# Kernel tuning notes

Measured on AMD Instinct MI355X. Metric: run time of the kernel, lower is better.

Reference implementation:

```python
import jax, jax.numpy as jnp
import numpy as np

N, D, K_FRAC = 4096, 256, 0.5
EPS = 1e-5  # BatchNorm1d default eps


def setup_inputs() -> dict:
    key = jax.random.key(0)
    kg, kh, kw = jax.random.split(key, 3)
    # sparse binary adjacency with self-loops so all degrees > 0 (pow(D,-1) finite)
    g = (jax.random.uniform(kg, (N, N)) < 0.004).astype(jnp.float32)
    g = jnp.maximum(g, jnp.eye(N, dtype=jnp.float32))
    h = jax.random.normal(kh, (N, D), dtype=jnp.float32)
    return {
        "g": g,
        "h": h,
        "gamma": jnp.ones((D,), jnp.float32),
        "beta": jnp.zeros((D,), jnp.float32),
        "w_proj": jax.random.normal(kw, (D, 1), dtype=jnp.float32) / np.sqrt(D),
        "b_proj": jnp.zeros((1,), jnp.float32),
        "sigma1": jnp.array([0.2], jnp.float32),
    }


def reference(g, h, gamma, beta, w_proj, b_proj, sigma1):
    # BatchNorm1d in training mode: batch statistics over the node axis
    mu = h.mean(0)
    var = h.var(0)  # biased variance, as torch uses for normalization
    h = (h - mu) / jnp.sqrt(var + EPS) * gamma + beta

    deg = g.sum(1)                               # [N] == Z2
    agg = (g @ h) / deg[:, None]                 # diag(D^-1) @ (g @ h), no NxN diag materialized
    Z1 = jnp.abs(h - agg).sum(1)                 # [N]
    pl = jax.nn.sigmoid(Z1 + deg)
    Z3 = (agg @ w_proj + b_proj)[:, 0]           # proj(Z3).squeeze()
    pg = jax.nn.softmax(Z3)                      # 1-D softmax (dim 0)
    pt = jax.nn.sigmoid(pl + pg)
    pf = jax.nn.sigmoid((h @ w_proj + b_proj)[:, 0])
    scores = sigma1[0] * pt + (1.0 - sigma1[0]) * pf

    # top_k_graph
    k = max(2, int(K_FRAC * N))
    _, idx = jax.lax.top_k(scores, k)            # [k]
    h_att = scores[:, None] * h                  # score-weighted features
    un_g = (g != 0).astype(jnp.float32)
    two_hop = ((un_g @ un_g) != 0).astype(jnp.float32)  # binarized 2-hop adjacency
    a_hat = two_hop[idx, :]                      # [k, N] row gather
    new_h = a_hat @ h_att                        # [k, D]
    g_new = a_hat[:, idx]                        # [k, k] column gather
    # norm_g: torch broadcast divides COLUMN j by row-sum degrees[j]
    g_new = g_new / g_new.sum(1)
    return g_new, new_h, idx
```

## Files before the change

### kernel.cpp

```cpp
#include <hip/hip_runtime.h>
#include <math.h>

#define NN 4096
#define DD 256
#define KK 2048
#define NW 64
#define SK 4
#define KC (NN / SK)
#define KW (KC / 32)

typedef float f32x4  __attribute__((ext_vector_type(4)));
typedef short bf16x8 __attribute__((ext_vector_type(8)));

__device__ __forceinline__ int build_list(const unsigned long long* __restrict__ B, int r,
                                          int l, int* cols, int cap) {
    unsigned long long word = B[(size_t)r * NW + l];
    int pc = __popcll(word);
    int off = pc;
    for (int d = 1; d < 64; d <<= 1) {
        int n = __shfl_up(off, d);
        if (l >= d) off += n;
    }
    int total = __shfl(off, 63);
    int base = off - pc;
    while (word) {
        int b = (int)__ffsll(word) - 1;
        word &= word - 1;
        if (base < cap) cols[base] = l * 64 + b;
        ++base;
    }
    return total;
}

__global__ void k_pre(const float* __restrict__ h, const float* __restrict__ g,
                      double* __restrict__ psum, double* __restrict__ psq,
                      unsigned long long* __restrict__ B) {
    int blk = blockIdx.x;
    int t = threadIdx.x;
    if (blk < 64) {
        int d = t;
        int r0 = blk * 64;
        double s0=0,s1=0,s2=0,s3=0,q0=0,q1=0,q2=0,q3=0;
        for (int k = 0; k < 64; k += 4) {
            double x0 = (double)h[(size_t)(r0+k+0) * DD + d];
            double x1 = (double)h[(size_t)(r0+k+1) * DD + d];
            double x2 = (double)h[(size_t)(r0+k+2) * DD + d];
            double x3 = (double)h[(size_t)(r0+k+3) * DD + d];
            s0 += x0; q0 += x0*x0;
            s1 += x1; q1 += x1*x1;
            s2 += x2; q2 += x2*x2;
            s3 += x3; q3 += x3*x3;
        }
        psum[blk * DD + d] = (s0+s1)+(s2+s3);
        psq [blk * DD + d] = (q0+q1)+(q2+q3);
    } else {
        int i = blk - 64;
        int q = t >> 6, l = t & 63;
        const float* gr = g + (size_t)i * NN;
        unsigned long long word = 0ull;
        int lw = l & 15;
        #pragma unroll
        for (int wi = 0; wi < 16; ++wi) {
            float v = gr[(q * 16 + wi) * 64 + l];
            unsigned long long m = __ballot(v != 0.0f);
            if (wi == lw) word = m;
        }
        if (l < 16) B[(size_t)i * NW + q * 16 + l] = word;
    }
}

__global__ void k_stats_final(const double* __restrict__ psum, const double* __restrict__ psq,
                              double* __restrict__ mu, double* __restrict__ rstd) {
    __shared__ double rs[4][DD];
    __shared__ double rq[4][DD];
    int t = threadIdx.x;
    int d = t & (DD - 1);
    int q = t >> 8;
    double s0=0,s1=0,q0=0,q1=0;
    int b0 = q * 16;
    for (int k = 0; k < 16; k += 2) {
        s0 += psum[(b0+k)   * DD + d];
        s1 += psum[(b0+k+1) * DD + d];
        q0 += psq [(b0+k)   * DD + d];
        q1 += psq [(b0+k+1) * DD + d];
    }
    rs[q][d] = s0 + s1;
    rq[q][d] = q0 + q1;
    __syncthreads();
    if (q == 0) {
        double S  = (rs[0][d]+rs[1][d]) + (rs[2][d]+rs[3][d]);
        double Q  = (rq[0][d]+rq[1][d]) + (rq[2][d]+rq[3][d]);
        double m  = S / (double)NN;
        double var = Q / (double)NN - m * m;
        mu[d]   = m;
        rstd[d] = 1.0 / sqrt(var + 1e-5);
    }
}

__global__ void k_main(const float* __restrict__ h, const double* __restrict__ mu,
                       const double* __restrict__ rstd, const float* __restrict__ gamma,
                       const float* __restrict__ beta, const unsigned long long* __restrict__ Bm,
                       const float* __restrict__ w, const float* __restrict__ bp,
                       float* __restrict__ hn, double* __restrict__ zpf,
                       unsigned long long* __restrict__ T, double* __restrict__ Z1,
                       double* __restrict__ Z3, int* __restrict__ degi) {
    __shared__ int cols[4][136];
    int blk = blockIdx.x;
    int t = threadIdx.x;
    int wv = t >> 6, l = t & 63;
    int r = blk * 4 + wv;
    int cnt = build_list(Bm, r, l, cols[wv], 128);
    if (cnt > 128) cnt = 128;
    const float4* h4 = (const float4*)h;
    double s0=0,s1=0,s2=0,s3=0,u0=0,u1=0,u2=0,u3=0;
    unsigned long long a0 = 0ull, a1 = 0ull;
    int j = 0;
    for (; j + 1 < cnt; j += 2) {
        int c0 = cols[wv][j], c1 = cols[wv][j + 1];
        float4 v0 = h4[(size_t)c0 * 64 + l];
        float4 v1 = h4[(size_t)c1 * 64 + l];
        a0 |= Bm[(size_t)c0 * NW + l];
        a1 |= Bm[(size_t)c1 * NW + l];
        s0 += (double)v0.x; s1 += (double)v0.y; s2 += (double)v0.z; s3 += (double)v0.w;
        u0 += (double)v1.x; u1 += (double)v1.y; u2 += (double)v1.z; u3 += (double)v1.w;
    }
    if (j < cnt) {
        int c0 = cols[wv][j];
        float4 v0 = h4[(size_t)c0 * 64 + l];
        a0 |= Bm[(size_t)c0 * NW + l];
        s0 += (double)v0.x; s1 += (double)v0.y; s2 += (double)v0.z; s3 += (double)v0.w;
    }
    T[(size_t)r * NW + l] = a0 | a1;
    s0 += u0; s1 += u1; s2 += u2; s3 += u3;
    const double2* mu2 = (const double2*)mu;
    const double2* rs2 = (const double2*)rstd;
    const float4*  ga4 = (const float4*)gamma;
    const float4*  be4 = (const float4*)beta;
    const float4*  w4  = (const float4*)w;
    double2 mA = mu2[2*l], mB = mu2[2*l+1];
    double2 rA = rs2[2*l], rB = rs2[2*l+1];
    float4 ga = ga4[l], be = be4[l], wl = w4[l];
    double inv = 1.0 / (double)cnt;
    double g0 = (s0 * inv - mA.x) * rA.x * (double)ga.x + (double)be.x;
    double g1 = (s1 * inv - mA.y) * rA.y * (double)ga.y + (double)be.y;
    double g2 = (s2 * inv - mB.x) * rB.x * (double)ga.z + (double)be.z;
    double g3 = (s3 * inv - mB.y) * rB.y * (double)ga.w + (double)be.w;
    float4 hv = h4[(size_t)r * 64 + l];
    double h0 = ((double)hv.x - mA.x) * rA.x * (double)ga.x + (double)be.x;
    double h1 = ((double)hv.y - mA.y) * rA.y * (double)ga.y + (double)be.y;
    double h2 = ((double)hv.z - mB.x) * rB.x * (double)ga.z + (double)be.z;
    double h3 = ((double)hv.w - mB.y) * rB.y * (double)ga.w + (double)be.w;
    float4 o = { (float)h0, (float)h1, (float)h2, (float)h3 };
    ((float4*)hn)[(size_t)r * 64 + l] = o;
    double z1p = (fabs(h0 - g0) + fabs(h1 - g1)) + (fabs(h2 - g2) + fabs(h3 - g3));
    double z3p = (g0 * (double)wl.x + g1 * (double)wl.y)
               + (g2 * (double)wl.z + g3 * (double)wl.w);
    double zfp = (h0 * (double)wl.x + h1 * (double)wl.y)
               + (h2 * (double)wl.z + h3 * (double)wl.w);
    for (int off = 32; off > 0; off >>= 1) {
        z1p += __shfl_down(z1p, off);
        z3p += __shfl_down(z3p, off);
        zfp += __shfl_down(zfp, off);
    }
    if (l == 0) {
        Z1[r] = z1p;
        Z3[r] = z3p + (double)bp[0];
        zpf[r] = zfp + (double)bp[0];
        degi[r] = cnt;
    }
}

__global__ void k_scorekeys(const double* __restrict__ Z1, const double* __restrict__ Z3,
                            const double* __restrict__ zpf, const int* __restrict__ degi,
                            const float* __restrict__ sigma1, float* __restrict__ scores,
                            unsigned long long* __restrict__ keys) {
    __shared__ double red[256];
    int t = threadIdx.x;
    double mx = -1e300;
    for (int k = 0; k < 16; ++k) mx = fmax(mx, Z3[t + 256 * k]);
    red[t] = mx;
    __syncthreads();
    for (int s = 128; s > 0; s >>= 1) {
        if (t < s) red[t] = fmax(red[t], red[t + s]);
        __syncthreads();
    }
    double M = red[0];
    __syncthreads();
    double se = 0.0;
    for (int k = 0; k < 16; ++k) se += exp(Z3[t + 256 * k] - M);
    red[t] = se;
    __syncthreads();
    for (int s = 128; s > 0; s >>= 1) {
        if (t < s) red[t] += red[t + s];
        __syncthreads();
    }
    double sum = red[0];
    int i = blockIdx.x * 256 + t;
    double s1 = (double)sigma1[0];
    double pg = exp(Z3[i] - M) / sum;
    double pl = 1.0 / (1.0 + exp(-(Z1[i] + (double)degi[i])));
    double pt = 1.0 / (1.0 + exp(-(pl + pg)));
    double pf = 1.0 / (1.0 + exp(-zpf[i]));
    float sc = (float)(s1 * pt + (1.0 - s1) * pf);
    scores[i] = sc;
    unsigned int b2 = __float_as_uint(sc);
    unsigned int ka = (b2 & 0x80000000u) ? ~b2 : (b2 ^ 0x80000000u);
    keys[i] = ((unsigned long long)(~ka) << 32) | (unsigned int)i;
}

__global__ void k_rank(const unsigned long long* __restrict__ keys, int* __restrict__ idx_int,
                       float* __restrict__ out_idx) {
    __shared__ unsigned long long Kl[NN];
    int t = threadIdx.x;
    for (int i = t; i < NN; i += 256) Kl[i] = keys[i];
    __syncthreads();
    int il = t >> 4, sub = t & 15;
    int i = blockIdx.x * 16 + il;
    unsigned long long ki = Kl[i];
    int c0 = 0, c1 = 0, c2 = 0, c3 = 0;
    for (int jj = 0; jj < 256; jj += 4) {
        int j = sub + (jj << 4);
        c0 += (Kl[j]      < ki) ? 1 : 0;
        c1 += (Kl[j + 16] < ki) ? 1 : 0;
        c2 += (Kl[j + 32] < ki) ? 1 : 0;
        c3 += (Kl[j + 48] < ki) ? 1 : 0;
    }
    int cnt = (c0 + c1) + (c2 + c3);
    for (int off = 8; off > 0; off >>= 1) cnt += __shfl_down(cnt, off, 16);
    if (sub == 0 && cnt < KK) {
        idx_int[cnt] = i;
        out_idx[cnt] = (float)i;
    }
}

__global__ void k_mid(const unsigned long long* __restrict__ T, const int* __restrict__ idx_int,
                      const float* __restrict__ scores, const float* __restrict__ hn,
                      float* __restrict__ inv_rs, unsigned short* __restrict__ haT_hi,
                      unsigned short* __restrict__ haT_lo) {
    int blk = blockIdx.x;
    int t = threadIdx.x;
    if (blk < 128) {
        __shared__ unsigned long long Sl[NW];
        if (t < NW) Sl[t] = 0ull;
        __syncthreads();
        for (int j = t; j < KK; j += 256) {
            int ii = idx_int[j];
            atomicOr(&Sl[ii >> 6], 1ull << (ii & 63));
        }
        __syncthreads();
        int wv = t >> 6, l = t & 63;
        unsigned long long sw = Sl[l];
        #pragma unroll
        for (int k = 0; k < 4; ++k) {
            int j = blk * 16 + wv * 4 + k;
            int r = idx_int[j];
            int c = (int)__popcll(T[(size_t)r * NW + l] & sw);
            for (int off = 32; off > 0; off >>= 1) c += __shfl_down(c, off);
            if (l == 0) inv_rs[j] = 1.0f / (float)c;
        }
    } else {
        int bb = blk - 128;
        int ng = bb & 63, dq = bb >> 6;
        int wv = t >> 6, l = t & 63;
        int node = ng * 64 + l;
        float sc = scores[node];
        const float* hr = hn + (size_t)node * DD;
        for (int d = dq * 64 + wv; d < (dq + 1) * 64; d += 4) {
            float x = hr[d] * sc;
            unsigned int xb = __float_as_uint(x);
            unsigned int hb = xb & 0xFFFF0000u;
            float lo = x - __uint_as_float(hb);
            unsigned int lb = __float_as_uint(lo);
            haT_hi[(size_t)d * NN + node] = (unsigned short)(hb >> 16);
            haT_lo[(size_t)d * NN + node] = (unsigned short)(lb >> 16);
        }
    }
}

__global__ void __launch_bounds__(256, 1)
k_nh(const unsigned long long* __restrict__ T, const int* __restrict__ idx_int,
     const unsigned short* __restrict__ haT_hi, const unsigned short* __restrict__ haT_lo,
     float* __restrict__ part) {
    __shared__ int ids[128];
    __shared__ unsigned int Ab[128][KW + 1];
    int blk = blockIdx.x;
    int rs = blk & 15, cb = (blk >> 4) & 3, kc = blk >> 6;
    int t = threadIdx.x;
    if (t < 128) ids[t] = idx_int[rs * 128 + t];
    __syncthreads();
    for (int i = t; i < 128 * KW; i += 256) {
        int row = i >> 5, w = i & (KW - 1);
        Ab[row][w] = ((const unsigned int*)(T + (size_t)ids[row] * NW))[kc * KW + w];
    }
    __syncthreads();
    int wv = t >> 6, l = t & 63;
    int lm = l & 15, lg = l >> 4;
    int row_base = (wv & 1) * 64;
    int col_base = cb * 64 + (wv >> 1) * 32;
    f32x4 acc[4][2];
    #pragma unroll
    for (int m = 0; m < 4; ++m) { acc[m][0] = (f32x4)0.0f; acc[m][1] = (f32x4)0.0f; }
    const unsigned short* ph0 = haT_hi + (size_t)(col_base + lm) * NN + kc * KC + lg * 8;
    const unsigned short* ph1 = ph0 + (size_t)16 * NN;
    const unsigned short* pl0 = haT_lo + (size_t)(col_base + lm) * NN + kc * KC + lg * 8;
    const unsigned short* pl1 = pl0 + (size_t)16 * NN;
    #pragma unroll 2
    for (int ks = 0; ks < KW; ++ks) {
        bf16x8 bh0 = *(const bf16x8*)(ph0 + ks * 32);
        bf16x8 bh1 = *(const bf16x8*)(ph1 + ks * 32);
        bf16x8 bl0 = *(const bf16x8*)(pl0 + ks * 32);
        bf16x8 bl1 = *(const bf16x8*)(pl1 + ks * 32);
        #pragma unroll
        for (int m = 0; m < 4; ++m) {
            unsigned int bits = Ab[row_base + m * 16 + lm][ks];
            unsigned int b8 = (bits >> (8 * lg)) & 0xFFu;
            union { unsigned int u[4]; bf16x8 v; } au;
            au.u[0] = ((b8 & 1u)        ? 0x3F80u : 0u) | ((b8 & 2u)   ? 0x3F800000u : 0u);
            au.u[1] = (((b8 >> 2) & 1u) ? 0x3F80u : 0u) | ((b8 & 8u)   ? 0x3F800000u : 0u);
            au.u[2] = (((b8 >> 4) & 1u) ? 0x3F80u : 0u) | ((b8 & 32u)  ? 0x3F800000u : 0u);
            au.u[3] = (((b8 >> 6) & 1u) ? 0x3F80u : 0u) | ((b8 & 128u) ? 0x3F800000u : 0u);
            bf16x8 a = au.v;
            acc[m][0] = __builtin_amdgcn_mfma_f32_16x16x32_bf16(a, bh0, acc[m][0], 0, 0, 0);
            acc[m][1] = __builtin_amdgcn_mfma_f32_16x16x32_bf16(a, bh1, acc[m][1], 0, 0, 0);
            acc[m][0] = __builtin_amdgcn_mfma_f32_16x16x32_bf16(a, bl0, acc[m][0], 0, 0, 0);
            acc[m][1] = __builtin_amdgcn_mfma_f32_16x16x32_bf16(a, bl1, acc[m][1], 0, 0, 0);
        }
    }
    float* pp = part + (size_t)kc * ((size_t)KK * DD);
    #pragma unroll
    for (int m = 0; m < 4; ++m) {
        int row0 = rs * 128 + row_base + m * 16 + lg * 4;
        #pragma unroll
        for (int n = 0; n < 2; ++n) {
            int col = col_base + n * 16 + lm;
            #pragma unroll
            for (int r = 0; r < 4; ++r)
                pp[(size_t)(row0 + r) * DD + col] = acc[m][n][r];
        }
    }
}

__global__ void k_out(const unsigned long long* __restrict__ T, const int* __restrict__ idx_int,
                      const float* __restrict__ inv_rs, const float* __restrict__ part,
                      float* __restrict__ out_gnew, float* __restrict__ out_newh) {
    __shared__ unsigned long long Tl[NW];
    int blk = blockIdx.x;
    int t = threadIdx.x;
    if (blk < KK) {
        int r = blk;
        if (t < NW) Tl[t] = T[(size_t)idx_int[r] * NW + t];
        __syncthreads();
        const int4*   idx4 = (const int4*)idx_int;
        const float4* irs4 = (const float4*)inv_rs;
        float4* out4 = (float4*)(out_gnew + (size_t)r * KK);
        for (int c4 = t; c4 < KK / 4; c4 += 256) {
            int4 jc = idx4[c4];
            float4 iv = irs4[c4];
            float4 o;
            o.x = ((Tl[jc.x >> 6] >> (jc.x & 63)) & 1ull) ? iv.x : 0.0f;
            o.y = ((Tl[jc.y >> 6] >> (jc.y & 63)) & 1ull) ? iv.y : 0.0f;
            o.z = ((Tl[jc.z >> 6] >> (jc.z & 63)) & 1ull) ? iv.z : 0.0f;
            o.w = ((Tl[jc.w >> 6] >> (jc.w & 63)) & 1ull) ? iv.w : 0.0f;
            out4[c4] = o;
        }
    } else {
        size_t off = (size_t)(blk - KK) * 1024 + (size_t)t * 4;
        const size_t stride = (size_t)KK * DD;
        float4 s0 = *(const float4*)(part + off);
        float4 s1 = *(const float4*)(part + off + stride);
        float4 s2 = *(const float4*)(part + off + 2 * stride);
        float4 s3 = *(const float4*)(part + off + 3 * stride);
        float4 o;
        o.x = (s0.x + s1.x) + (s2.x + s3.x);
        o.y = (s0.y + s1.y) + (s2.y + s3.y);
        o.z = (s0.z + s1.z) + (s2.z + s3.z);
        o.w = (s0.w + s1.w) + (s2.w + s3.w);
        *(float4*)(out_newh + off) = o;
    }
}

extern "C" void kernel_launch(void* const* d_in, const int* in_sizes, int n_in,
                              void* d_out, int out_size, void* d_ws, size_t ws_size,
                              hipStream_t stream) {
    const float* g      = (const float*)d_in[0];
    const float* h      = (const float*)d_in[1];
    const float* gamma  = (const float*)d_in[2];
    const float* beta   = (const float*)d_in[3];
    const float* w_proj = (const float*)d_in[4];
    const float* b_proj = (const float*)d_in[5];
    const float* sigma1 = (const float*)d_in[6];

    char* p = (char*)d_ws;
    auto alloc = [&](size_t bytes) -> void* {
        void* q = (void*)p;
        p += (bytes + 255) & ~(size_t)255;
        return q;
    };
    double* mu      = (double*)alloc(DD * 8);
    double* rstd    = (double*)alloc(DD * 8);
    double* psum    = (double*)alloc(64 * DD * 8);
    double* psq     = (double*)alloc(64 * DD * 8);
    double* zpf     = (double*)alloc(NN * 8);
    double* Z1      = (double*)alloc(NN * 8);
    double* Z3      = (double*)alloc(NN * 8);
    int*    degi    = (int*)alloc(NN * 4);
    float*  scores  = (float*)alloc(NN * 4);
    unsigned long long* keys = (unsigned long long*)alloc(NN * 8);
    int*    idx_int = (int*)alloc(KK * 4);
    float*  inv_rs  = (float*)alloc(KK * 4);
    unsigned long long* B = (unsigned long long*)alloc((size_t)NN * NW * 8);
    unsigned long long* T = (unsigned long long*)alloc((size_t)NN * NW * 8);
    float*  hn      = (float*)alloc((size_t)NN * DD * 4);
    unsigned short* haT_hi = (unsigned short*)alloc((size_t)DD * NN * 2);
    unsigned short* haT_lo = (unsigned short*)alloc((size_t)DD * NN * 2);
    float*  part    = (float*)alloc((size_t)SK * KK * DD * 4);

    float* out_gnew = (float*)d_out;
    float* out_newh = out_gnew + (size_t)KK * KK;
    float* out_idx  = out_newh + (size_t)KK * DD;

    hipLaunchKernelGGL(k_pre,         dim3(64 + NN), dim3(256),  0, stream, h, g, psum, psq, B);
    hipLaunchKernelGGL(k_stats_final, dim3(1),       dim3(1024), 0, stream, psum, psq, mu, rstd);
    hipLaunchKernelGGL(k_main,        dim3(1024),    dim3(256),  0, stream, h, mu, rstd, gamma, beta, B, w_proj, b_proj, hn, zpf, T, Z1, Z3, degi);
    hipLaunchKernelGGL(k_scorekeys,   dim3(16),      dim3(256),  0, stream, Z1, Z3, zpf, degi, sigma1, scores, keys);
    hipLaunchKernelGGL(k_rank,        dim3(256),     dim3(256),  0, stream, keys, idx_int, out_idx);
    hipLaunchKernelGGL(k_mid,         dim3(128 + 256), dim3(256), 0, stream, T, idx_int, scores, hn, inv_rs, haT_hi, haT_lo);
    hipLaunchKernelGGL(k_nh,          dim3(256),     dim3(256),  0, stream, T, idx_int, haT_hi, haT_lo, part);
    hipLaunchKernelGGL(k_out,         dim3(KK + 512), dim3(256), 0, stream, T, idx_int, inv_rs, part, out_gnew, out_newh);
}
```

Baseline: 171.0 us.

## Fuse all stages into one persistent cooperative kernel with grid syncs

Replaces the eight separate kernel launches with a single cooperative persistent kernel. Each former kernel becomes a grid-stride phase, phases are separated by grid-wide barriers, and shared memory is held in a union. The aim is to remove launch overhead and the gaps between the many small dependent kernels. In exchange, grid size is capped by occupancy, so large phases such as the adjacency bitmask build and the output write run with fewer blocks. Each grid sync also adds its own cost, and the MFMA phase now runs under a 4-blocks-per-CU launch bound where it previously had 1.

```diff
diff --git a/kernel.cpp b/kernel.cpp
--- a/kernel.cpp
+++ b/kernel.cpp
@@ -1,5 +1,8 @@
 #include <hip/hip_runtime.h>
+#include <hip/hip_cooperative_groups.h>
 #include <math.h>
+
+namespace cg = cooperative_groups;
 
 #define NN 4096
 #define DD 256
@@ -11,6 +14,15 @@
 
 typedef float f32x4  __attribute__((ext_vector_type(4)));
 typedef short bf16x8 __attribute__((ext_vector_type(8)));
+
+union SmemU {
+    unsigned long long keys[NN];
+    struct { int cols[4][136]; } mn;
+    struct { double red[256]; } sk;
+    struct { int ids[128]; unsigned int Ab[128][KW + 1]; } nh;
+    struct { unsigned long long Sl[NW]; } mid;
+    struct { unsigned long long Tl[NW]; } og;
+};
 
 __device__ __forceinline__ int build_list(const unsigned long long* __restrict__ B, int r,
                                           int l, int* cols, int cap) {
@@ -32,14 +44,31 @@
     return total;
 }
 
-__global__ void k_pre(const float* __restrict__ h, const float* __restrict__ g,
-                      double* __restrict__ psum, double* __restrict__ psq,
-                      unsigned long long* __restrict__ B) {
-    int blk = blockIdx.x;
-    int t = threadIdx.x;
-    if (blk < 64) {
+__global__ void __launch_bounds__(256, 4)
+k_fused(const float* __restrict__ g, const float* __restrict__ h,
+        const float* __restrict__ gamma, const float* __restrict__ beta,
+        const float* __restrict__ w, const float* __restrict__ bp,
+        const float* __restrict__ sigma1,
+        double* __restrict__ psum, double* __restrict__ psq,
+        double* __restrict__ mu, double* __restrict__ rstd,
+        unsigned long long* __restrict__ B, unsigned long long* __restrict__ T,
+        float* __restrict__ hn, double* __restrict__ zpf,
+        double* __restrict__ Z1, double* __restrict__ Z3, int* __restrict__ degi,
+        float* __restrict__ scores, unsigned long long* __restrict__ keys,
+        int* __restrict__ idx_int, float* __restrict__ out_idx, float* __restrict__ inv_rs,
+        unsigned short* __restrict__ haT_hi, unsigned short* __restrict__ haT_lo,
+        float* __restrict__ part, float* __restrict__ out_gnew, float* __restrict__ out_newh)
+{
+    cg::grid_group gg = cg::this_grid();
+    __shared__ SmemU sm;
+    const int NB  = gridDim.x;
+    const int bid = blockIdx.x;
+    const int t   = threadIdx.x;
+    const int wv  = t >> 6, l = t & 63;
+
+    for (int vb = bid; vb < 64; vb += NB) {
         int d = t;
-        int r0 = blk * 64;
+        int r0 = vb * 64;
         double s0=0,s1=0,s2=0,s3=0,q0=0,q1=0,q2=0,q3=0;
         for (int k = 0; k < 64; k += 4) {
             double x0 = (double)h[(size_t)(r0+k+0) * DD + d];
@@ -51,331 +80,291 @@
             s2 += x2; q2 += x2*x2;
             s3 += x3; q3 += x3*x3;
         }
-        psum[blk * DD + d] = (s0+s1)+(s2+s3);
-        psq [blk * DD + d] = (q0+q1)+(q2+q3);
-    } else {
-        int i = blk - 64;
-        int q = t >> 6, l = t & 63;
+        psum[vb * DD + d] = (s0+s1)+(s2+s3);
+        psq [vb * DD + d] = (q0+q1)+(q2+q3);
+    }
+    for (int i = bid; i < NN; i += NB) {
         const float* gr = g + (size_t)i * NN;
         unsigned long long word = 0ull;
         int lw = l & 15;
         #pragma unroll
         for (int wi = 0; wi < 16; ++wi) {
-            float v = gr[(q * 16 + wi) * 64 + l];
+            float v = gr[(wv * 16 + wi) * 64 + l];
             unsigned long long m = __ballot(v != 0.0f);
             if (wi == lw) word = m;
         }
-        if (l < 16) B[(size_t)i * NW + q * 16 + l] = word;
-    }
-}
-
-__global__ void k_stats_final(const double* __restrict__ psum, const double* __restrict__ psq,
-                              double* __restrict__ mu, double* __restrict__ rstd) {
-    __shared__ double rs[4][DD];
-    __shared__ double rq[4][DD];
-    int t = threadIdx.x;
-    int d = t & (DD - 1);
-    int q = t >> 8;
-    double s0=0,s1=0,q0=0,q1=0;
-    int b0 = q * 16;
-    for (int k = 0; k < 16; k += 2) {
-        s0 += psum[(b0+k)   * DD + d];
-        s1 += psum[(b0+k+1) * DD + d];
-        q0 += psq [(b0+k)   * DD + d];
-        q1 += psq [(b0+k+1) * DD + d];
-    }
-    rs[q][d] = s0 + s1;
-    rq[q][d] = q0 + q1;
-    __syncthreads();
-    if (q == 0) {
-        double S  = (rs[0][d]+rs[1][d]) + (rs[2][d]+rs[3][d]);
-        double Q  = (rq[0][d]+rq[1][d]) + (rq[2][d]+rq[3][d]);
-        double m  = S / (double)NN;
+        if (l < 16) B[(size_t)i * NW + wv * 16 + l] = word;
+    }
+    gg.sync();
+
+    if (bid == 0) {
+        int d = t;
+        double S = 0.0, Q = 0.0;
+        for (int k = 0; k < 64; ++k) {
+            S += psum[k * DD + d];
+            Q += psq [k * DD + d];
+        }
+        double m   = S / (double)NN;
         double var = Q / (double)NN - m * m;
         mu[d]   = m;
         rstd[d] = 1.0 / sqrt(var + 1e-5);
     }
-}
-
-__global__ void k_main(const float* __restrict__ h, const double* __restrict__ mu,
-                       const double* __restrict__ rstd, const float* __restrict__ gamma,
-                       const float* __restrict__ beta, const unsigned long long* __restrict__ Bm,
-                       const float* __restrict__ w, const float* __restrict__ bp,
-                       float* __restrict__ hn, double* __restrict__ zpf,
-                       unsigned long long* __restrict__ T, double* __restrict__ Z1,
-                       double* __restrict__ Z3, int* __restrict__ degi) {
-    __shared__ int cols[4][136];
-    int blk = blockIdx.x;
-    int t = threadIdx.x;
-    int wv = t >> 6, l = t & 63;
-    int r = blk * 4 + wv;
-    int cnt = build_list(Bm, r, l, cols[wv], 128);
-    if (cnt > 128) cnt = 128;
-    const float4* h4 = (const float4*)h;
-    double s0=0,s1=0,s2=0,s3=0,u0=0,u1=0,u2=0,u3=0;
-    unsigned long long a0 = 0ull, a1 = 0ull;
-    int j = 0;
-    for (; j + 1 < cnt; j += 2) {
-        int c0 = cols[wv][j], c1 = cols[wv][j + 1];
-        float4 v0 = h4[(size_t)c0 * 64 + l];
-        float4 v1 = h4[(size_t)c1 * 64 + l];
-        a0 |= Bm[(size_t)c0 * NW + l];
-        a1 |= Bm[(size_t)c1 * NW + l];
-        s0 += (double)v0.x; s1 += (double)v0.y; s2 += (double)v0.z; s3 += (double)v0.w;
-        u0 += (double)v1.x; u1 += (double)v1.y; u2 += (double)v1.z; u3 += (double)v1.w;
-    }
-    if (j < cnt) {
-        int c0 = cols[wv][j];
-        float4 v0 = h4[(size_t)c0 * 64 + l];
-        a0 |= Bm[(size_t)c0 * NW + l];
-        s0 += (double)v0.x; s1 += (double)v0.y; s2 += (double)v0.z; s3 += (double)v0.w;
-    }
-    T[(size_t)r * NW + l] = a0 | a1;
-    s0 += u0; s1 += u1; s2 += u2; s3 += u3;
-    const double2* mu2 = (const double2*)mu;
-    const double2* rs2 = (const double2*)rstd;
-    const float4*  ga4 = (const float4*)gamma;
-    const float4*  be4 = (const float4*)beta;
-    const float4*  w4  = (const float4*)w;
-    double2 mA = mu2[2*l], mB = mu2[2*l+1];
-    double2 rA = rs2[2*l], rB = rs2[2*l+1];
-    float4 ga = ga4[l], be = be4[l], wl = w4[l];
-    double inv = 1.0 / (double)cnt;
-    double g0 = (s0 * inv - mA.x) * rA.x * (double)ga.x + (double)be.x;
-    double g1 = (s1 * inv - mA.y) * rA.y * (double)ga.y + (double)be.y;
-    double g2 = (s2 * inv - mB.x) * rB.x * (double)ga.z + (double)be.z;
-    double g3 = (s3 * inv - mB.y) * rB.y * (double)ga.w + (double)be.w;
-    float4 hv = h4[(size_t)r * 64 + l];
-    double h0 = ((double)hv.x - mA.x) * rA.x * (double)ga.x + (double)be.x;
-    double h1 = ((double)hv.y - mA.y) * rA.y * (double)ga.y + (double)be.y;
-    double h2 = ((double)hv.z - mB.x) * rB.x * (double)ga.z + (double)be.z;
-    double h3 = ((double)hv.w - mB.y) * rB.y * (double)ga.w + (double)be.w;
-    float4 o = { (float)h0, (float)h1, (float)h2, (float)h3 };
-    ((float4*)hn)[(size_t)r * 64 + l] = o;
-    double z1p = (fabs(h0 - g0) + fabs(h1 - g1)) + (fabs(h2 - g2) + fabs(h3 - g3));
-    double z3p = (g0 * (double)wl.x + g1 * (double)wl.y)
-               + (g2 * (double)wl.z + g3 * (double)wl.w);
-    double zfp = (h0 * (double)wl.x + h1 * (double)wl.y)
-               + (h2 * (double)wl.z + h3 * (double)wl.w);
-    for (int off = 32; off > 0; off >>= 1) {
-        z1p += __shfl_down(z1p, off);
-        z3p += __shfl_down(z3p, off);
-        zfp += __shfl_down(zfp, off);
-    }
-    if (l == 0) {
-        Z1[r] = z1p;
-        Z3[r] = z3p + (double)bp[0];
-        zpf[r] = zfp + (double)bp[0];
-        degi[r] = cnt;
-    }
-}
-
-__global__ void k_scorekeys(const double* __restrict__ Z1, const double* __restrict__ Z3,
-                            const double* __restrict__ zpf, const int* __restrict__ degi,
-                            const float* __restrict__ sigma1, float* __restrict__ scores,
-                            unsigned long long* __restrict__ keys) {
-    __shared__ double red[256];
-    int t = threadIdx.x;
-    double mx = -1e300;
-    for (int k = 0; k < 16; ++k) mx = fmax(mx, Z3[t + 256 * k]);
-    red[t] = mx;
-    __syncthreads();
-    for (int s = 128; s > 0; s >>= 1) {
-        if (t < s) red[t] = fmax(red[t], red[t + s]);
+    gg.sync();
+
+    for (int vb = bid; vb < NN / 4; vb += NB) {
+        int r = vb * 4 + wv;
+        int* cols = sm.mn.cols[wv];
+        int cnt = build_list(B, r, l, cols, 128);
+        if (cnt > 128) cnt = 128;
+        const float4* h4 = (const float4*)h;
+        double s0=0,s1=0,s2=0,s3=0,u0=0,u1=0,u2=0,u3=0;
+        unsigned long long a0 = 0ull, a1 = 0ull;
+        int j = 0;
+        for (; j + 1 < cnt; j += 2) {
+            int c0 = cols[j], c1 = cols[j + 1];
+            float4 v0 = h4[(size_t)c0 * 64 + l];
+            float4 v1 = h4[(size_t)c1 * 64 + l];
+            a0 |= B[(size_t)c0 * NW + l];
+            a1 |= B[(size_t)c1 * NW + l];
+            s0 += (double)v0.x; s1 += (double)v0.y; s2 += (double)v0.z; s3 += (double)v0.w;
+            u0 += (double)v1.x; u1 += (double)v1.y; u2 += (double)v1.z; u3 += (double)v1.w;
+        }
+        if (j < cnt) {
+            int c0 = cols[j];
+            float4 v0 = h4[(size_t)c0 * 64 + l];
+            a0 |= B[(size_t)c0 * NW + l];
+            s0 += (double)v0.x; s1 += (double)v0.y; s2 += (double)v0.z; s3 += (double)v0.w;
+        }
+        T[(size_t)r * NW + l] = a0 | a1;
+        s0 += u0; s1 += u1; s2 += u2; s3 += u3;
+        const double2* mu2 = (const double2*)mu;
+        const double2* rs2 = (const double2*)rstd;
+        const float4*  ga4 = (const float4*)gamma;
+        const float4*  be4 = (const float4*)beta;
+        const float4*  w4  = (const float4*)w;
+        double2 mA = mu2[2*l], mB = mu2[2*l+1];
+        double2 rA = rs2[2*l], rB = rs2[2*l+1];
+        float4 ga = ga4[l], be = be4[l], wl = w4[l];
+        double inv = 1.0 / (double)cnt;
+        double g0 = (s0 * inv - mA.x) * rA.x * (double)ga.x + (double)be.x;
+        double g1 = (s1 * inv - mA.y) * rA.y * (double)ga.y + (double)be.y;
+        double g2 = (s2 * inv - mB.x) * rB.x * (double)ga.z + (double)be.z;
+        double g3 = (s3 * inv - mB.y) * rB.y * (double)ga.w + (double)be.w;
+        float4 hv = h4[(size_t)r * 64 + l];
+        double h0 = ((double)hv.x - mA.x) * rA.x * (double)ga.x + (double)be.x;
+        double h1 = ((double)hv.y - mA.y) * rA.y * (double)ga.y + (double)be.y;
+        double h2 = ((double)hv.z - mB.x) * rB.x * (double)ga.z + (double)be.z;
+        double h3 = ((double)hv.w - mB.y) * rB.y * (double)ga.w + (double)be.w;
+        float4 o = { (float)h0, (float)h1, (float)h2, (float)h3 };
+        ((float4*)hn)[(size_t)r * 64 + l] = o;
+        double z1p = (fabs(h0 - g0) + fabs(h1 - g1)) + (fabs(h2 - g2) + fabs(h3 - g3));
+        double z3p = (g0 * (double)wl.x + g1 * (double)wl.y)
+                   + (g2 * (double)wl.z + g3 * (double)wl.w);
+        double zfp = (h0 * (double)wl.x + h1 * (double)wl.y)
+                   + (h2 * (double)wl.z + h3 * (double)wl.w);
+        for (int off = 32; off > 0; off >>= 1) {
+            z1p += __shfl_down(z1p, off);
+            z3p += __shfl_down(z3p, off);
+            zfp += __shfl_down(zfp, off);
+        }
+        if (l == 0) {
+            Z1[r] = z1p;
+            Z3[r] = z3p + (double)bp[0];
+            zpf[r] = zfp + (double)bp[0];
+            degi[r] = cnt;
+        }
+    }
+    gg.sync();
+
+    for (int vb = bid; vb < 16; vb += NB) {
+        double* red = sm.sk.red;
+        double mx = -1e300;
+        for (int k = 0; k < 16; ++k) mx = fmax(mx, Z3[t + 256 * k]);
+        red[t] = mx;
         __syncthreads();
-    }
-    double M = red[0];
-    __syncthreads();
-    double se = 0.0;
-    for (int k = 0; k < 16; ++k) se += exp(Z3[t + 256 * k] - M);
-    red[t] = se;
-    __syncthreads();
-    for (int s = 128; s > 0; s >>= 1) {
-        if (t < s) red[t] += red[t + s];
+        for (int s = 128; s > 0; s >>= 1) {
+            if (t < s) red[t] = fmax(red[t], red[t + s]);
+            __syncthreads();
+        }
+        double M = red[0];
         __syncthreads();
-    }
-    double sum = red[0];
-    int i = blockIdx.x * 256 + t;
-    double s1 = (double)sigma1[0];
-    double pg = exp(Z3[i] - M) / sum;
-    double pl = 1.0 / (1.0 + exp(-(Z1[i] + (double)degi[i])));
-    double pt = 1.0 / (1.0 + exp(-(pl + pg)));
-    double pf = 1.0 / (1.0 + exp(-zpf[i]));
-    float sc = (float)(s1 * pt + (1.0 - s1) * pf);
-    scores[i] = sc;
-    unsigned int b2 = __float_as_uint(sc);
-    unsigned int ka = (b2 & 0x80000000u) ? ~b2 : (b2 ^ 0x80000000u);
-    keys[i] = ((unsigned long long)(~ka) << 32) | (unsigned int)i;
-}
-
-__global__ void k_rank(const unsigned long long* __restrict__ keys, int* __restrict__ idx_int,
-                       float* __restrict__ out_idx) {
-    __shared__ unsigned long long Kl[NN];
-    int t = threadIdx.x;
-    for (int i = t; i < NN; i += 256) Kl[i] = keys[i];
-    __syncthreads();
-    int il = t >> 4, sub = t & 15;
-    int i = blockIdx.x * 16 + il;
-    unsigned long long ki = Kl[i];
-    int c0 = 0, c1 = 0, c2 = 0, c3 = 0;
-    for (int jj = 0; jj < 256; jj += 4) {
-        int j = sub + (jj << 4);
-        c0 += (Kl[j]      < ki) ? 1 : 0;
-        c1 += (Kl[j + 16] < ki) ? 1 : 0;
-        c2 += (Kl[j + 32] < ki) ? 1 : 0;
-        c3 += (Kl[j + 48] < ki) ? 1 : 0;
-    }
-    int cnt = (c0 + c1) + (c2 + c3);
-    for (int off = 8; off > 0; off >>= 1) cnt += __shfl_down(cnt, off, 16);
-    if (sub == 0 && cnt < KK) {
-        idx_int[cnt] = i;
-        out_idx[cnt] = (float)i;
-    }
-}
-
-__global__ void k_mid(const unsigned long long* __restrict__ T, const int* __restrict__ idx_int,
-                      const float* __restrict__ scores, const float* __restrict__ hn,
-                      float* __restrict__ inv_rs, unsigned short* __restrict__ haT_hi,
-                      unsigned short* __restrict__ haT_lo) {
-    int blk = blockIdx.x;
-    int t = threadIdx.x;
-    if (blk < 128) {
-        __shared__ unsigned long long Sl[NW];
-        if (t < NW) Sl[t] = 0ull;
+        double se = 0.0;
+        for (int k = 0; k < 16; ++k) se += exp(Z3[t + 256 * k] - M);
+        red[t] = se;
         __syncthreads();
-        for (int j = t; j < KK; j += 256) {
-            int ii = idx_int[j];
-            atomicOr(&Sl[ii >> 6], 1ull << (ii & 63));
-        }
+        for (int s = 128; s > 0; s >>= 1) {
+            if (t < s) red[t] += red[t + s];
+            __syncthreads();
+        }
+        double sum = red[0];
+        int i = vb * 256 + t;
+        double s1 = (double)sigma1[0];
+        double pg = exp(Z3[i] - M) / sum;
+        double pl = 1.0 / (1.0 + exp(-(Z1[i] + (double)degi[i])));
+        double pt = 1.0 / (1.0 + exp(-(pl + pg)));
+        double pf = 1.0 / (1.0 + exp(-zpf[i]));
+        float sc = (float)(s1 * pt + (1.0 - s1) * pf);
+        scores[i] = sc;
+        unsigned int b2 = __float_as_uint(sc);
+        unsigned int ka = (b2 & 0x80000000u) ? ~b2 : (b2 ^ 0x80000000u);
+        keys[i] = ((unsigned long long)(~ka) << 32) | (unsigned int)i;
         __syncthreads();
-        int wv = t >> 6, l = t & 63;
-        unsigned long long sw = Sl[l];
-        #pragma unroll
-        for (int k = 0; k < 4; ++k) {
-            int j = blk * 16 + wv * 4 + k;
-            int r = idx_int[j];
-            int c = (int)__popcll(T[(size_t)r * NW + l] & sw);
-            for (int off = 32; off > 0; off >>= 1) c += __shfl_down(c, off);
-            if (l == 0) inv_rs[j] = 1.0f / (float)c;
-        }
-    } else {
-        int bb = blk - 128;
-        int ng = bb & 63, dq = bb >> 6;
-        int wv = t >> 6, l = t & 63;
-        int node = ng * 64 + l;
-        float sc = scores[node];
-        const float* hr = hn + (size_t)node * DD;
-        for (int d = dq * 64 + wv; d < (dq + 1) * 64; d += 4) {
-            float x = hr[d] * sc;
-            unsigned int xb = __float_as_uint(x);
-            unsigned int hb = xb & 0xFFFF0000u;
-            float lo = x - __uint_as_float(hb);
-            unsigned int lb = __float_as_uint(lo);
-            haT_hi[(size_t)d * NN + node] = (unsigned short)(hb >> 16);
-            haT_lo[(size_t)d * NN + node] = (unsigned short)(lb >> 16);
-        }
-    }
-}
-
-__global__ void __launch_bounds__(256, 1)
-k_nh(const unsigned long long* __restrict__ T, const int* __restrict__ idx_int,
-     const unsigned short* __restrict__ haT_hi, const unsigned short* __restrict__ haT_lo,
-     float* __restrict__ part) {
-    __shared__ int ids[128];
-    __shared__ unsigned int Ab[128][KW + 1];
-    int blk = blockIdx.x;
-    int rs = blk & 15, cb = (blk >> 4) & 3, kc = blk >> 6;
-    int t = threadIdx.x;
-    if (t < 128) ids[t] = idx_int[rs * 128 + t];
-    __syncthreads();
-    for (int i = t; i < 128 * KW; i += 256) {
-        int row = i >> 5, w = i & (KW - 1);
-        Ab[row][w] = ((const unsigned int*)(T + (size_t)ids[row] * NW))[kc * KW + w];
-    }
-    __syncthreads();
-    int wv = t >> 6, l = t & 63;
-    int lm = l & 15, lg = l >> 4;
-    int row_base = (wv & 1) * 64;
-    int col_base = cb * 64 + (wv >> 1) * 32;
-    f32x4 acc[4][2];
-    #pragma unroll
-    for (int m = 0; m < 4; ++m) { acc[m][0] = (f32x4)0.0f; acc[m][1] = (f32x4)0.0f; }
-    const unsigned short* ph0 = haT_hi + (size_t)(col_base + lm) * NN + kc * KC + lg * 8;
-    const unsigned short* ph1 = ph0 + (size_t)16 * NN;
-    const unsigned short* pl0 = haT_lo + (size_t)(col_base + lm) * NN + kc * KC + lg * 8;
-    const unsigned short* pl1 = pl0 + (size_t)16 * NN;
-    #pragma unroll 2
-    for (int ks = 0; ks < KW; ++ks) {
-        bf16x8 bh0 = *(const bf16x8*)(ph0 + ks * 32);
-        bf16x8 bh1 = *(const bf16x8*)(ph1 + ks * 32);
-        bf16x8 bl0 = *(const bf16x8*)(pl0 + ks * 32);
-        bf16x8 bl1 = *(const bf16x8*)(pl1 + ks * 32);
-        #pragma unroll
-        for (int m = 0; m < 4; ++m) {
-            unsigned int bits = Ab[row_base + m * 16 + lm][ks];
-            unsigned int b8 = (bits >> (8 * lg)) & 0xFFu;
-            union { unsigned int u[4]; bf16x8 v; } au;
-            au.u[0] = ((b8 & 1u)        ? 0x3F80u : 0u) | ((b8 & 2u)   ? 0x3F800000u : 0u);
-            au.u[1] = (((b8 >> 2) & 1u) ? 0x3F80u : 0u) | ((b8 & 8u)   ? 0x3F800000u : 0u);
-            au.u[2] = (((b8 >> 4) & 1u) ? 0x3F80u : 0u) | ((b8 & 32u)  ? 0x3F800000u : 0u);
-            au.u[3] = (((b8 >> 6) & 1u) ? 0x3F80u : 0u) | ((b8 & 128u) ? 0x3F800000u : 0u);
-            bf16x8 a = au.v;
-            acc[m][0] = __builtin_amdgcn_mfma_f32_16x16x32_bf16(a, bh0, acc[m][0], 0, 0, 0);
-            acc[m][1] = __builtin_amdgcn_mfma_f32_16x16x32_bf16(a, bh1, acc[m][1], 0, 0, 0);
-            acc[m][0] = __builtin_amdgcn_mfma_f32_16x16x32_bf16(a, bl0, acc[m][0], 0, 0, 0);
-            acc[m][1] = __builtin_amdgcn_mfma_f32_16x16x32_bf16(a, bl1, acc[m][1], 0, 0, 0);
-        }
-    }
-    float* pp = part + (size_t)kc * ((size_t)KK * DD);
-    #pragma unroll
-    for (int m = 0; m < 4; ++m) {
-        int row0 = rs * 128 + row_base + m * 16 + lg * 4;
-        #pragma unroll
-        for (int n = 0; n < 2; ++n) {
-            int col = col_base + n * 16 + lm;
+    }
+    gg.sync();
+
+    for (int vb = bid; vb < 512; vb += NB) {
+        if (vb < 256) {
+            for (int i = t; i < NN; i += 256) sm.keys[i] = keys[i];
+            __syncthreads();
+            int il = t >> 4, sub = t & 15;
+            int i = vb * 16 + il;
+            unsigned long long ki = sm.keys[i];
+            int c0 = 0, c1 = 0, c2 = 0, c3 = 0;
+            for (int jj = 0; jj < 256; jj += 4) {
+                int jx = sub + (jj << 4);
+                c0 += (sm.keys[jx]      < ki) ? 1 : 0;
+                c1 += (sm.keys[jx + 16] < ki) ? 1 : 0;
+                c2 += (sm.keys[jx + 32] < ki) ? 1 : 0;
+                c3 += (sm.keys[jx + 48] < ki) ? 1 : 0;
+            }
+            int cnt = (c0 + c1) + (c2 + c3);
+            for (int off = 8; off > 0; off >>= 1) cnt += __shfl_down(cnt, off, 16);
+            if (sub == 0 && cnt < KK) {
+                idx_int[cnt] = i;
+                out_idx[cnt] = (float)i;
+            }
+            __syncthreads();
+        } else {
+            int bb = vb - 256;
+            int ng = bb & 63, dq = bb >> 6;
+            int node = ng * 64 + l;
+            float sc = scores[node];
+            const float* hr = hn + (size_t)node * DD;
+            for (int d = dq * 64 + wv; d < (dq + 1) * 64; d += 4) {
+                float x = hr[d] * sc;
+                unsigned int xb = __float_as_uint(x);
+                unsigned int hb = xb & 0xFFFF0000u;
+                float lo = x - __uint_as_float(hb);
+                unsigned int lb = __float_as_uint(lo);
+                haT_hi[(size_t)d * NN + node] = (unsigned short)(hb >> 16);
+                haT_lo[(size_t)d * NN + node] = (unsigned short)(lb >> 16);
+            }
+        }
+    }
+    gg.sync();
+
+    for (int vb = bid; vb < 384; vb += NB) {
+        if (vb < 128) {
+            if (t < NW) sm.mid.Sl[t] = 0ull;
+            __syncthreads();
+            for (int j = t; j < KK; j += 256) {
+                int ii = idx_int[j];
+                atomicOr(&sm.mid.Sl[ii >> 6], 1ull << (ii & 63));
+            }
+            __syncthreads();
+            unsigned long long sw = sm.mid.Sl[l];
             #pragma unroll
-            for (int r = 0; r < 4; ++r)
-                pp[(size_t)(row0 + r) * DD + col] = acc[m][n][r];
-        }
-    }
-}
-
-__global__ void k_out(const unsigned long long* __restrict__ T, const int* __restrict__ idx_int,
-                      const float* __restrict__ inv_rs, const float* __restrict__ part,
-                      float* __restrict__ out_gnew, float* __restrict__ out_newh) {
-    __shared__ unsigned long long Tl[NW];
-    int blk = blockIdx.x;
-    int t = threadIdx.x;
-    if (blk < KK) {
-        int r = blk;
-        if (t < NW) Tl[t] = T[(size_t)idx_int[r] * NW + t];
-        __syncthreads();
-        const int4*   idx4 = (const int4*)idx_int;
-        const float4* irs4 = (const float4*)inv_rs;
-        float4* out4 = (float4*)(out_gnew + (size_t)r * KK);
-        for (int c4 = t; c4 < KK / 4; c4 += 256) {
-            int4 jc = idx4[c4];
-            float4 iv = irs4[c4];
+            for (int k = 0; k < 4; ++k) {
+                int j = vb * 16 + wv * 4 + k;
+                int r = idx_int[j];
+                int c = (int)__popcll(T[(size_t)r * NW + l] & sw);
+                for (int off = 32; off > 0; off >>= 1) c += __shfl_down(c, off);
+                if (l == 0) inv_rs[j] = 1.0f / (float)c;
+            }
+            __syncthreads();
+        } else {
+            int blk = vb - 128;
+            int rs = blk & 15, cb = (blk >> 4) & 3, kc = blk >> 6;
+            if (t < 128) sm.nh.ids[t] = idx_int[rs * 128 + t];
+            __syncthreads();
+            for (int i = t; i < 128 * KW; i += 256) {
+                int row = i >> 5, wd = i & (KW - 1);
+                sm.nh.Ab[row][wd] =
+                    ((const unsigned int*)(T + (size_t)sm.nh.ids[row] * NW))[kc * KW + wd];
+            }
+            __syncthreads();
+            int lm = l & 15, lg = l >> 4;
+            int row_base = (wv & 1) * 64;
+            int col_base = cb * 64 + (wv >> 1) * 32;
+            f32x4 acc[4][2];
+            #pragma unroll
+            for (int m = 0; m < 4; ++m) { acc[m][0] = (f32x4)0.0f; acc[m][1] = (f32x4)0.0f; }
+            const unsigned short* ph0 = haT_hi + (size_t)(col_base + lm) * NN + kc * KC + lg * 8;
+            const unsigned short* ph1 = ph0 + (size_t)16 * NN;
+            const unsigned short* pl0 = haT_lo + (size_t)(col_base + lm) * NN + kc * KC + lg * 8;
+            const unsigned short* pl1 = pl0 + (size_t)16 * NN;
+            #pragma unroll 2
+            for (int ks = 0; ks < KW; ++ks) {
+                bf16x8 bh0 = *(const bf16x8*)(ph0 + ks * 32);
+                bf16x8 bh1 = *(const bf16x8*)(ph1 + ks * 32);
+                bf16x8 bl0 = *(const bf16x8*)(pl0 + ks * 32);
+                bf16x8 bl1 = *(const bf16x8*)(pl1 + ks * 32);
+                #pragma unroll
+                for (int m = 0; m < 4; ++m) {
+                    unsigned int bits = sm.nh.Ab[row_base + m * 16 + lm][ks];
+                    unsigned int b8 = (bits >> (8 * lg)) & 0xFFu;
+                    union { unsigned int u[4]; bf16x8 v; } au;
+                    au.u[0] = ((b8 & 1u)        ? 0x3F80u : 0u) | ((b8 & 2u)   ? 0x3F800000u : 0u);
+                    au.u[1] = (((b8 >> 2) & 1u) ? 0x3F80u : 0u) | ((b8 & 8u)   ? 0x3F800000u : 0u);
+                    au.u[2] = (((b8 >> 4) & 1u) ? 0x3F80u : 0u) | ((b8 & 32u)  ? 0x3F800000u : 0u);
+                    au.u[3] = (((b8 >> 6) & 1u) ? 0x3F80u : 0u) | ((b8 & 128u) ? 0x3F800000u : 0u);
+                    bf16x8 a = au.v;
+                    acc[m][0] = __builtin_amdgcn_mfma_f32_16x16x32_bf16(a, bh0, acc[m][0], 0, 0, 0);
+                    acc[m][1] = __builtin_amdgcn_mfma_f32_16x16x32_bf16(a, bh1, acc[m][1], 0, 0, 0);
+                    acc[m][0] = __builtin_amdgcn_mfma_f32_16x16x32_bf16(a, bl0, acc[m][0], 0, 0, 0);
+                    acc[m][1] = __builtin_amdgcn_mfma_f32_16x16x32_bf16(a, bl1, acc[m][1], 0, 0, 0);
+                }
+            }
+            float* pp = part + (size_t)kc * ((size_t)KK * DD);
+            #pragma unroll
+            for (int m = 0; m < 4; ++m) {
+                int row0 = rs * 128 + row_base + m * 16 + lg * 4;
+                #pragma unroll
+                for (int n = 0; n < 2; ++n) {
+                    int col = col_base + n * 16 + lm;
+                    #pragma unroll
+                    for (int rr = 0; rr < 4; ++rr)
+                        pp[(size_t)(row0 + rr) * DD + col] = acc[m][n][rr];
+                }
+            }
+            __syncthreads();
+        }
+    }
+    gg.sync();
+
+    for (int vb = bid; vb < KK + 512; vb += NB) {
+        if (vb < KK) {
+            int r = vb;
+            if (t < NW) sm.og.Tl[t] = T[(size_t)idx_int[r] * NW + t];
+            __syncthreads();
+            const int4*   idx4 = (const int4*)idx_int;
+            const float4* irs4 = (const float4*)inv_rs;
+            float4* out4 = (float4*)(out_gnew + (size_t)r * KK);
+            for (int c4 = t; c4 < KK / 4; c4 += 256) {
+                int4 jc = idx4[c4];
+                float4 iv = irs4[c4];
+                float4 o;
+                o.x = ((sm.og.Tl[jc.x >> 6] >> (jc.x & 63)) & 1ull) ? iv.x : 0.0f;
+                o.y = ((sm.og.Tl[jc.y >> 6] >> (jc.y & 63)) & 1ull) ? iv.y : 0.0f;
+                o.z = ((sm.og.Tl[jc.z >> 6] >> (jc.z & 63)) & 1ull) ? iv.z : 0.0f;
+                o.w = ((sm.og.Tl[jc.w >> 6] >> (jc.w & 63)) & 1ull) ? iv.w : 0.0f;
+                out4[c4] = o;
+            }
+            __syncthreads();
+        } else {
+            size_t off = (size_t)(vb - KK) * 1024 + (size_t)t * 4;
+            const size_t stride = (size_t)KK * DD;
+            float4 s0 = *(const float4*)(part + off);
+            float4 s1 = *(const float4*)(part + off + stride);
+            float4 s2 = *(const float4*)(part + off + 2 * stride);
+            float4 s3 = *(const float4*)(part + off + 3 * stride);
             float4 o;
-            o.x = ((Tl[jc.x >> 6] >> (jc.x & 63)) & 1ull) ? iv.x : 0.0f;
-            o.y = ((Tl[jc.y >> 6] >> (jc.y & 63)) & 1ull) ? iv.y : 0.0f;
-            o.z = ((Tl[jc.z >> 6] >> (jc.z & 63)) & 1ull) ? iv.z : 0.0f;
-            o.w = ((Tl[jc.w >> 6] >> (jc.w & 63)) & 1ull) ? iv.w : 0.0f;
-            out4[c4] = o;
-        }
-    } else {
-        size_t off = (size_t)(blk - KK) * 1024 + (size_t)t * 4;
-        const size_t stride = (size_t)KK * DD;
-        float4 s0 = *(const float4*)(part + off);
-        float4 s1 = *(const float4*)(part + off + stride);
-        float4 s2 = *(const float4*)(part + off + 2 * stride);
-        float4 s3 = *(const float4*)(part + off + 3 * stride);
-        float4 o;
-        o.x = (s0.x + s1.x) + (s2.x + s3.x);
-        o.y = (s0.y + s1.y) + (s2.y + s3.y);
-        o.z = (s0.z + s1.z) + (s2.z + s3.z);
-        o.w = (s0.w + s1.w) + (s2.w + s3.w);
-        *(float4*)(out_newh + off) = o;
+            o.x = (s0.x + s1.x) + (s2.x + s3.x);
+            o.y = (s0.y + s1.y) + (s2.y + s3.y);
+            o.z = (s0.z + s1.z) + (s2.z + s3.z);
+            o.w = (s0.w + s1.w) + (s2.w + s3.w);
+            *(float4*)(out_newh + off) = o;
+        }
     }
 }
 
@@ -419,12 +408,24 @@
     float* out_newh = out_gnew + (size_t)KK * KK;
     float* out_idx  = out_newh + (size_t)KK * DD;
 
-    hipLaunchKernelGGL(k_pre,         dim3(64 + NN), dim3(256),  0, stream, h, g, psum, psq, B);
-    hipLaunchKernelGGL(k_stats_final, dim3(1),       dim3(1024), 0, stream, psum, psq, mu, rstd);
-    hipLaunchKernelGGL(k_main,        dim3(1024),    dim3(256),  0, stream, h, mu, rstd, gamma, beta, B, w_proj, b_proj, hn, zpf, T, Z1, Z3, degi);
-    hipLaunchKernelGGL(k_scorekeys,   dim3(16),      dim3(256),  0, stream, Z1, Z3, zpf, degi, sigma1, scores, keys);
-    hipLaunchKernelGGL(k_rank,        dim3(256),     dim3(256),  0, stream, keys, idx_int, out_idx);
-    hipLaunchKernelGGL(k_mid,         dim3(128 + 256), dim3(256), 0, stream, T, idx_int, scores, hn, inv_rs, haT_hi, haT_lo);
-    hipLaunchKernelGGL(k_nh,          dim3(256),     dim3(256),  0, stream, T, idx_int, haT_hi, haT_lo, part);
-    hipLaunchKernelGGL(k_out,         dim3(KK + 512), dim3(256), 0, stream, T, idx_int, inv_rs, part, out_gnew, out_newh);
+    static int nblk = 0;
+    if (nblk == 0) {
+        int bpc = 0;
+        hipOccupancyMaxActiveBlocksPerMultiprocessor(&bpc, k_fused, 256, 0);
+        if (bpc < 1) bpc = 1;
+        long cap = (long)bpc * 256;
+        nblk = (int)(cap < 1024 ? cap : 1024);
+    }
+
+    void* args[] = {
+        (void*)&g, (void*)&h, (void*)&gamma, (void*)&beta, (void*)&w_proj,
+        (void*)&b_proj, (void*)&sigma1,
+        (void*)&psum, (void*)&psq, (void*)&mu, (void*)&rstd,
+        (void*)&B, (void*)&T, (void*)&hn, (void*)&zpf,
+        (void*)&Z1, (void*)&Z3, (void*)&degi,
+        (void*)&scores, (void*)&keys, (void*)&idx_int, (void*)&out_idx, (void*)&inv_rs,
+        (void*)&haT_hi, (void*)&haT_lo, (void*)&part,
+        (void*)&out_gnew, (void*)&out_newh
+    };
+    hipLaunchCooperativeKernel((const void*)k_fused, dim3(nblk), dim3(256), args, 0, stream);
 }
```

New measurement: 499.2 us. 192% more time.
